# Performance work log

Hardware: AMD Instinct MI355X
Metric: run time of the kernel (lower is better)

Reference implementation:

```python
import jax, jax.numpy as jnp
import numpy as np

N_OUT = 128
N_PARAMS = 64
DEGREE = 3
LB = -3.0
UB = 3.0
N_POINTS = 1048576


def get_knots():
    # (ub-lb) * [zeros(degree), linspace(0,1,n_params-degree), ones(degree)] + lb
    t = np.concatenate([np.zeros(DEGREE), np.linspace(0.0, 1.0, N_PARAMS - DEGREE), np.ones(DEGREE)])
    return jnp.asarray((UB - LB) * t + LB, dtype=jnp.float32)  # [n_params + degree]


def eval_basis(x, knots):
    # x: [N], knots: [n_knots] with n_knots = n_params + degree
    n_knots = knots.shape[0]
    xb = x[:, None]  # [N,1]
    # degree-0 indicator functions, vectorized over all knot intervals
    phis = ((knots[:-1] <= xb) & (xb < knots[1:])).astype(x.dtype)  # [N, n_knots-1]
    # Cox-de Boor recursion, vectorized over basis index i for each degree d
    for d in range(1, DEGREE + 1):
        m = n_knots - d - 1
        ld = knots[d:d + m] - knots[:m]          # left denominators  [m]
        rd = knots[d + 1:d + 1 + m] - knots[1:1 + m]  # right denominators [m]
        left = jnp.where(ld != 0, (xb - knots[:m]) / jnp.where(ld != 0, ld, 1.0), 0.0)
        right = jnp.where(rd != 0, (knots[d + 1:d + 1 + m] - xb) / jnp.where(rd != 0, rd, 1.0), 0.0)
        new = left * phis[:, :m] + right * phis[:, 1:m + 1]
        phis = jnp.concatenate([new, phis[:, m:]], axis=1)
    # last used column is replaced by SiLU(x) (column n_knots - degree - 1 == n_params - 1)
    phis = phis.at[:, n_knots - DEGREE - 1].set(jax.nn.silu(x))
    return phis[:, :N_PARAMS]  # [N, n_params]


def setup_inputs() -> dict:
    key = jax.random.key(0)
    k1, k2 = jax.random.split(key)
    x = jax.random.normal(k1, (N_POINTS,), dtype=jnp.float32)
    params = jax.random.normal(k2, (N_PARAMS, N_OUT), dtype=jnp.float32) * 0.1
    return {"x": x, "params": params}


def reference(x, params):
    knots = get_knots()
    basis = eval_basis(x, knots)          # [N, n_params]
    return (basis @ params).T             # [n_out, N]
```

## Files before the change

### kernel.cpp

```cpp
#include <hip/hip_runtime.h>

#define NPTS 1048576
#define NOUT 128
#define NPAR 64
#define BLOCK 256
#define PPT 2
#define STRH 136

typedef float vf2 __attribute__((ext_vector_type(2)));

__device__ __forceinline__ unsigned short f2bf(float f) {
    unsigned int u = __float_as_uint(f);
    u += 0x7fffu + ((u >> 16) & 1u);
    return (unsigned short)(u >> 16);
}

__device__ __forceinline__ void bf2x(unsigned int u, float& lo, float& hi) {
    lo = __uint_as_float(u << 16);
    hi = __uint_as_float(u & 0xffff0000u);
}

__global__ __launch_bounds__(BLOCK, 8)
void kan_kernel(const float* __restrict__ x,
                const float* __restrict__ params,
                float* __restrict__ out) {
    __shared__ unsigned short sH[NPAR * STRH];

    const int tid = threadIdx.x;

    {
        const float4* p4 = (const float4*)params;
        #pragma unroll
        for (int g = tid; g < NPAR * (NOUT / 4); g += BLOCK) {
            float4 v = p4[g];
            ushort4 h;
            h.x = f2bf(v.x); h.y = f2bf(v.y); h.z = f2bf(v.z); h.w = f2bf(v.w);
            *(ushort4*)&sH[(g >> 5) * STRH + (g & 31) * 4] = h;
        }
    }
    __syncthreads();

    const int base = blockIdx.x * (BLOCK * PPT) + tid * PPT;
    const float2 xv = *(const float2*)(x + base);
    float xs[PPT] = {xv.x, xv.y};

    float b[PPT][4];
    float sil[PPT];
    int   rbase[PPT];

    #pragma unroll
    for (int pp = 0; pp < PPT; ++pp) {
        float xx = xs[pp];
        sil[pp] = xx / (1.0f + __expf(-xx));

        float inr = (xx >= -3.0f && xx < 3.0f) ? 1.0f : 0.0f;
        float u = (xx + 3.0f) * 10.0f;
        int si = (int)u;
        si = si < 0 ? 0 : (si > 59 ? 59 : si);

        float Ki   = -3.0f + 0.1f * (float)si;
        float Kim1 = -3.0f + 0.1f * (float)(si - 1 > 0 ? si - 1 : 0);
        float Kim2 = -3.0f + 0.1f * (float)(si - 2 > 0 ? si - 2 : 0);
        float Kip1 = -3.0f + 0.1f * (float)(si + 1);
        float Kip2 = -3.0f + 0.1f * (float)(si + 2 < 60 ? si + 2 : 60);
        float Kip3 = -3.0f + 0.1f * (float)(si + 3 < 60 ? si + 3 : 60);

        float l1 = xx - Ki,   r1 = Kip1 - xx;
        float l2 = xx - Kim1, r2 = Kip2 - xx;
        float l3 = xx - Kim2, r3 = Kip3 - xx;

        float N0 = 1.0f, N1, N2, N3, t, saved;
        t = N0 / (r1 + l1); N0 = r1 * t; N1 = l1 * t;
        t = N0 / (r1 + l2); N0 = r1 * t;          saved = l2 * t;
        t = N1 / (r2 + l1); N1 = saved + r2 * t;  N2    = l1 * t;
        t = N0 / (r1 + l3); N0 = r1 * t;          saved = l3 * t;
        t = N1 / (r2 + l2); N1 = saved + r2 * t;  saved = l2 * t;
        t = N2 / (r3 + l1); N2 = saved + r3 * t;  N3    = l1 * t;

        b[pp][0] = N0 * inr;
        b[pp][1] = N1 * inr;
        b[pp][2] = N2 * inr;
        b[pp][3] = N3 * inr;
        rbase[pp] = si;
    }

    float* outc = out + base;

    #pragma unroll 1
    for (int j0 = 0; j0 < NOUT; j0 += 8) {
        uint4 u63 = *(const uint4*)&sH[63 * STRH + j0];
        float p63f[8];
        bf2x(u63.x, p63f[0], p63f[1]);
        bf2x(u63.y, p63f[2], p63f[3]);
        bf2x(u63.z, p63f[4], p63f[5]);
        bf2x(u63.w, p63f[6], p63f[7]);

        float a[PPT][8];
        #pragma unroll
        for (int pp = 0; pp < PPT; ++pp) {
            const unsigned short* rp = &sH[rbase[pp] * STRH + j0];
            float s = sil[pp];
            float acc[8];
            #pragma unroll
            for (int c = 0; c < 8; ++c) acc[c] = s * p63f[c];

            #pragma unroll
            for (int r = 0; r < 4; ++r) {
                uint4 q = *(const uint4*)(rp + r * STRH);
                float f[8];
                bf2x(q.x, f[0], f[1]); bf2x(q.y, f[2], f[3]);
                bf2x(q.z, f[4], f[5]); bf2x(q.w, f[6], f[7]);
                float br = b[pp][r];
                #pragma unroll
                for (int c = 0; c < 8; ++c) acc[c] = fmaf(br, f[c], acc[c]);
            }
            #pragma unroll
            for (int c = 0; c < 8; ++c) a[pp][c] = acc[c];
        }

        #pragma unroll
        for (int c = 0; c < 8; ++c) {
            vf2 v = { a[0][c], a[1][c] };
            __builtin_nontemporal_store(v, (vf2*)(outc + (size_t)(j0 + c) * NPTS));
        }
    }
}

extern "C" void kernel_launch(void* const* d_in, const int* in_sizes, int n_in,
                              void* d_out, int out_size, void* d_ws, size_t ws_size,
                              hipStream_t stream) {
    const float* x      = (const float*)d_in[0];
    const float* params = (const float*)d_in[1];
    float* out          = (float*)d_out;

    dim3 grid(NPTS / (BLOCK * PPT));
    kan_kernel<<<grid, BLOCK, 0, stream>>>(x, params, out);
}
```

Measured before the change: 120.7 us.

## Stage output tiles through shared memory for row-contiguous wide stores, 4 points per thread

Each thread now handles four points and writes its eight output values per group into a shared staging buffer. After a barrier, each wavefront copies two full output rows of 1024 contiguous floats to global memory with 16-byte stores. This replaces the earlier per-thread 8-byte nontemporal stores spread across rows, and also drops the nontemporal hint. The cost is two extra barriers per output group, 32 KB of extra shared memory per block, and a lower occupancy target in launch bounds.

```diff
diff --git a/kernel.cpp b/kernel.cpp
--- a/kernel.cpp
+++ b/kernel.cpp
@@ -4,10 +4,13 @@
 #define NOUT 128
 #define NPAR 64
 #define BLOCK 256
-#define PPT 2
+#define PPT 4
+#define CPB (BLOCK * PPT)
 #define STRH 136
+#define G 8
+#define SST 1024
 
-typedef float vf2 __attribute__((ext_vector_type(2)));
+typedef float vf4 __attribute__((ext_vector_type(4)));
 
 __device__ __forceinline__ unsigned short f2bf(float f) {
     unsigned int u = __float_as_uint(f);
@@ -20,11 +23,12 @@
     hi = __uint_as_float(u & 0xffff0000u);
 }
 
-__global__ __launch_bounds__(BLOCK, 8)
+__global__ __launch_bounds__(BLOCK, 4)
 void kan_kernel(const float* __restrict__ x,
                 const float* __restrict__ params,
                 float* __restrict__ out) {
     __shared__ unsigned short sH[NPAR * STRH];
+    __shared__ float sS[G * SST];
 
     const int tid = threadIdx.x;
 
@@ -38,11 +42,10 @@
             *(ushort4*)&sH[(g >> 5) * STRH + (g & 31) * 4] = h;
         }
     }
-    __syncthreads();
 
-    const int base = blockIdx.x * (BLOCK * PPT) + tid * PPT;
-    const float2 xv = *(const float2*)(x + base);
-    float xs[PPT] = {xv.x, xv.y};
+    const int base = blockIdx.x * CPB + tid * PPT;
+    const float4 xv = *(const float4*)(x + base);
+    float xs[PPT] = {xv.x, xv.y, xv.z, xv.w};
 
     float b[PPT][4];
     float sil[PPT];
@@ -84,10 +87,13 @@
         rbase[pp] = si;
     }
 
-    float* outc = out + base;
+    __syncthreads();
+
+    const int w = tid >> 6;
+    const int l = tid & 63;
 
     #pragma unroll 1
-    for (int j0 = 0; j0 < NOUT; j0 += 8) {
+    for (int j0 = 0; j0 < NOUT; j0 += G) {
         uint4 u63 = *(const uint4*)&sH[63 * STRH + j0];
         float p63f[8];
         bf2x(u63.x, p63f[0], p63f[1]);
@@ -120,9 +126,24 @@
 
         #pragma unroll
         for (int c = 0; c < 8; ++c) {
-            vf2 v = { a[0][c], a[1][c] };
-            __builtin_nontemporal_store(v, (vf2*)(outc + (size_t)(j0 + c) * NPTS));
+            vf4 v = { a[0][c], a[1][c], a[2][c], a[3][c] };
+            *(vf4*)&sS[c * SST + tid * 4] = v;
         }
+
+        __syncthreads();
+
+        #pragma unroll
+        for (int rr = 0; rr < 2; ++rr) {
+            const int r = 2 * w + rr;
+            float* orow = out + (size_t)(j0 + r) * NPTS + blockIdx.x * CPB;
+            #pragma unroll
+            for (int k = 0; k < 4; ++k) {
+                vf4 v = *(const vf4*)&sS[r * SST + k * 256 + l * 4];
+                *(vf4*)(orow + k * 256 + l * 4) = v;
+            }
+        }
+
+        __syncthreads();
     }
 }
 
@@ -133,6 +154,6 @@
     const float* params = (const float*)d_in[1];
     float* out          = (float*)d_out;
 
-    dim3 grid(NPTS / (BLOCK * PPT));
+    dim3 grid(NPTS / CPB);
     kan_kernel<<<grid, BLOCK, 0, stream>>>(x, params, out);
 }
```

Result: no change. 120.2 us (median of 3 runs) (-0.4%).

## Split work over output-row groups and point strips with wider stores

Applied to the files above, without the earlier changes.

The grid now runs over 8 groups of 16 output rows times 512 strips of 2048 points. Each block stages only its 16-column slice of params into a small shared buffer and processes 4 points per thread in two chunks, writing float4 stores without the nontemporal hint. The goal is less shared memory per block, fewer redundant param conversions, and wider coalesced writes. In exchange, the basis and SiLU computation is repeated once per output group (8 times per point), and launch bounds drop to 4 blocks per SM.

```diff
diff --git a/kernel.cpp b/kernel.cpp
--- a/kernel.cpp
+++ b/kernel.cpp
@@ -4,10 +4,13 @@
 #define NOUT 128
 #define NPAR 64
 #define BLOCK 256
-#define PPT 2
-#define STRH 136
+#define RPB 16
+#define NGRP (NOUT / RPB)
+#define PPB 2048
+#define STRIPS (NPTS / PPB)
+#define PROW 24
 
-typedef float vf2 __attribute__((ext_vector_type(2)));
+typedef float vf4 __attribute__((ext_vector_type(4)));
 
 __device__ __forceinline__ unsigned short f2bf(float f) {
     unsigned int u = __float_as_uint(f);
@@ -20,108 +23,105 @@
     hi = __uint_as_float(u & 0xffff0000u);
 }
 
-__global__ __launch_bounds__(BLOCK, 8)
+__global__ __launch_bounds__(BLOCK, 4)
 void kan_kernel(const float* __restrict__ x,
                 const float* __restrict__ params,
                 float* __restrict__ out) {
-    __shared__ unsigned short sH[NPAR * STRH];
+    __shared__ unsigned short sP[NPAR * PROW];
 
-    const int tid = threadIdx.x;
+    const int tid   = threadIdx.x;
+    const int g     = blockIdx.x >> 9;
+    const int strip = blockIdx.x & (STRIPS - 1);
+    const int j0    = g * RPB;
 
     {
-        const float4* p4 = (const float4*)params;
-        #pragma unroll
-        for (int g = tid; g < NPAR * (NOUT / 4); g += BLOCK) {
-            float4 v = p4[g];
-            ushort4 h;
-            h.x = f2bf(v.x); h.y = f2bf(v.y); h.z = f2bf(v.z); h.w = f2bf(v.w);
-            *(ushort4*)&sH[(g >> 5) * STRH + (g & 31) * 4] = h;
-        }
+        const int row  = tid >> 2;
+        const int quad = tid & 3;
+        float4 v = *(const float4*)(params + row * NOUT + j0 + quad * 4);
+        ushort4 h;
+        h.x = f2bf(v.x); h.y = f2bf(v.y); h.z = f2bf(v.z); h.w = f2bf(v.w);
+        *(ushort4*)&sP[row * PROW + quad * 4] = h;
     }
     __syncthreads();
 
-    const int base = blockIdx.x * (BLOCK * PPT) + tid * PPT;
-    const float2 xv = *(const float2*)(x + base);
-    float xs[PPT] = {xv.x, xv.y};
+    #pragma unroll 1
+    for (int ch = 0; ch < 2; ++ch) {
+        const int base = strip * PPB + ch * 1024 + tid * 4;
+        const float4 xv = *(const float4*)(x + base);
+        float xs[4] = {xv.x, xv.y, xv.z, xv.w};
 
-    float b[PPT][4];
-    float sil[PPT];
-    int   rbase[PPT];
+        float b[4][4], sil[4];
+        int rbase[4];
 
-    #pragma unroll
-    for (int pp = 0; pp < PPT; ++pp) {
-        float xx = xs[pp];
-        sil[pp] = xx / (1.0f + __expf(-xx));
+        #pragma unroll
+        for (int pp = 0; pp < 4; ++pp) {
+            float xx = xs[pp];
+            sil[pp] = xx / (1.0f + __expf(-xx));
 
-        float inr = (xx >= -3.0f && xx < 3.0f) ? 1.0f : 0.0f;
-        float u = (xx + 3.0f) * 10.0f;
-        int si = (int)u;
-        si = si < 0 ? 0 : (si > 59 ? 59 : si);
+            float inr = (xx >= -3.0f && xx < 3.0f) ? 1.0f : 0.0f;
+            float u = (xx + 3.0f) * 10.0f;
+            int si = (int)u;
+            si = si < 0 ? 0 : (si > 59 ? 59 : si);
 
-        float Ki   = -3.0f + 0.1f * (float)si;
-        float Kim1 = -3.0f + 0.1f * (float)(si - 1 > 0 ? si - 1 : 0);
-        float Kim2 = -3.0f + 0.1f * (float)(si - 2 > 0 ? si - 2 : 0);
-        float Kip1 = -3.0f + 0.1f * (float)(si + 1);
-        float Kip2 = -3.0f + 0.1f * (float)(si + 2 < 60 ? si + 2 : 60);
-        float Kip3 = -3.0f + 0.1f * (float)(si + 3 < 60 ? si + 3 : 60);
+            float Ki   = -3.0f + 0.1f * (float)si;
+            float Kim1 = -3.0f + 0.1f * (float)(si - 1 > 0 ? si - 1 : 0);
+            float Kim2 = -3.0f + 0.1f * (float)(si - 2 > 0 ? si - 2 : 0);
+            float Kip1 = -3.0f + 0.1f * (float)(si + 1);
+            float Kip2 = -3.0f + 0.1f * (float)(si + 2 < 60 ? si + 2 : 60);
+            float Kip3 = -3.0f + 0.1f * (float)(si + 3 < 60 ? si + 3 : 60);
 
-        float l1 = xx - Ki,   r1 = Kip1 - xx;
-        float l2 = xx - Kim1, r2 = Kip2 - xx;
-        float l3 = xx - Kim2, r3 = Kip3 - xx;
+            float l1 = xx - Ki,   r1 = Kip1 - xx;
+            float l2 = xx - Kim1, r2 = Kip2 - xx;
+            float l3 = xx - Kim2, r3 = Kip3 - xx;
 
-        float N0 = 1.0f, N1, N2, N3, t, saved;
-        t = N0 / (r1 + l1); N0 = r1 * t; N1 = l1 * t;
-        t = N0 / (r1 + l2); N0 = r1 * t;          saved = l2 * t;
-        t = N1 / (r2 + l1); N1 = saved + r2 * t;  N2    = l1 * t;
-        t = N0 / (r1 + l3); N0 = r1 * t;          saved = l3 * t;
-        t = N1 / (r2 + l2); N1 = saved + r2 * t;  saved = l2 * t;
-        t = N2 / (r3 + l1); N2 = saved + r3 * t;  N3    = l1 * t;
+            float N0 = 1.0f, N1, N2, N3, t, saved;
+            t = N0 / (r1 + l1); N0 = r1 * t; N1 = l1 * t;
+            t = N0 / (r1 + l2); N0 = r1 * t;          saved = l2 * t;
+            t = N1 / (r2 + l1); N1 = saved + r2 * t;  N2    = l1 * t;
+            t = N0 / (r1 + l3); N0 = r1 * t;          saved = l3 * t;
+            t = N1 / (r2 + l2); N1 = saved + r2 * t;  saved = l2 * t;
+            t = N2 / (r3 + l1); N2 = saved + r3 * t;  N3    = l1 * t;
 
-        b[pp][0] = N0 * inr;
-        b[pp][1] = N1 * inr;
-        b[pp][2] = N2 * inr;
-        b[pp][3] = N3 * inr;
-        rbase[pp] = si;
-    }
-
-    float* outc = out + base;
-
-    #pragma unroll 1
-    for (int j0 = 0; j0 < NOUT; j0 += 8) {
-        uint4 u63 = *(const uint4*)&sH[63 * STRH + j0];
-        float p63f[8];
-        bf2x(u63.x, p63f[0], p63f[1]);
-        bf2x(u63.y, p63f[2], p63f[3]);
-        bf2x(u63.z, p63f[4], p63f[5]);
-        bf2x(u63.w, p63f[6], p63f[7]);
-
-        float a[PPT][8];
-        #pragma unroll
-        for (int pp = 0; pp < PPT; ++pp) {
-            const unsigned short* rp = &sH[rbase[pp] * STRH + j0];
-            float s = sil[pp];
-            float acc[8];
-            #pragma unroll
-            for (int c = 0; c < 8; ++c) acc[c] = s * p63f[c];
-
-            #pragma unroll
-            for (int r = 0; r < 4; ++r) {
-                uint4 q = *(const uint4*)(rp + r * STRH);
-                float f[8];
-                bf2x(q.x, f[0], f[1]); bf2x(q.y, f[2], f[3]);
-                bf2x(q.z, f[4], f[5]); bf2x(q.w, f[6], f[7]);
-                float br = b[pp][r];
-                #pragma unroll
-                for (int c = 0; c < 8; ++c) acc[c] = fmaf(br, f[c], acc[c]);
-            }
-            #pragma unroll
-            for (int c = 0; c < 8; ++c) a[pp][c] = acc[c];
+            b[pp][0] = N0 * inr;
+            b[pp][1] = N1 * inr;
+            b[pp][2] = N2 * inr;
+            b[pp][3] = N3 * inr;
+            rbase[pp] = si;
         }
 
         #pragma unroll
-        for (int c = 0; c < 8; ++c) {
-            vf2 v = { a[0][c], a[1][c] };
-            __builtin_nontemporal_store(v, (vf2*)(outc + (size_t)(j0 + c) * NPTS));
+        for (int h = 0; h < 2; ++h) {
+            uint4 u63 = *(const uint4*)&sP[63 * PROW + h * 8];
+            float p63f[8];
+            bf2x(u63.x, p63f[0], p63f[1]); bf2x(u63.y, p63f[2], p63f[3]);
+            bf2x(u63.z, p63f[4], p63f[5]); bf2x(u63.w, p63f[6], p63f[7]);
+
+            float a[4][8];
+            #pragma unroll
+            for (int pp = 0; pp < 4; ++pp) {
+                float s = sil[pp];
+                float acc[8];
+                #pragma unroll
+                for (int c = 0; c < 8; ++c) acc[c] = s * p63f[c];
+                #pragma unroll
+                for (int r = 0; r < 4; ++r) {
+                    uint4 q = *(const uint4*)&sP[(rbase[pp] + r) * PROW + h * 8];
+                    float f[8];
+                    bf2x(q.x, f[0], f[1]); bf2x(q.y, f[2], f[3]);
+                    bf2x(q.z, f[4], f[5]); bf2x(q.w, f[6], f[7]);
+                    float br = b[pp][r];
+                    #pragma unroll
+                    for (int c = 0; c < 8; ++c) acc[c] = fmaf(br, f[c], acc[c]);
+                }
+                #pragma unroll
+                for (int c = 0; c < 8; ++c) a[pp][c] = acc[c];
+            }
+
+            #pragma unroll
+            for (int c = 0; c < 8; ++c) {
+                vf4 v = { a[0][c], a[1][c], a[2][c], a[3][c] };
+                *(vf4*)(out + (size_t)(j0 + h * 8 + c) * NPTS + base) = v;
+            }
         }
     }
 }
@@ -133,6 +133,6 @@
     const float* params = (const float*)d_in[1];
     float* out          = (float*)d_out;
 
-    dim3 grid(NPTS / (BLOCK * PPT));
+    dim3 grid(NGRP * STRIPS);
     kan_kernel<<<grid, BLOCK, 0, stream>>>(x, params, out);
 }
```

New measurement: 183.0 us. 1.52x slower.
